# Kernel tuning notes

Measured on AMD Instinct MI355X. Metric: run time of the kernel, lower is better.

Reference implementation:

```python
import jax, jax.numpy as jnp
import numpy as np

NL, D, H, DH, DFF, DIN, MAXLEN = 3, 128, 4, 32, 512, 64, 4096
B, L = 2, 2048


def setup_inputs() -> dict:
    key = jax.random.key(0)
    ks = jax.random.split(key, 10)
    def n(k, shape, s=0.02):
        return jax.random.normal(k, shape, jnp.float32) * s
    return dict(
        x=jax.random.normal(ks[0], (B, L, DIN), jnp.float32),
        embed_w=n(ks[1], (D, DIN)), embed_b=jnp.zeros((D,), jnp.float32),
        pos_emb=n(ks[2], (MAXLEN + 1, D)),
        cls=n(ks[3], (1, 1, D)),
        in_proj_w=n(ks[4], (NL, 3 * D, D)), in_proj_b=jnp.zeros((NL, 3 * D), jnp.float32),
        out_w=n(ks[5], (NL, D, D)), out_b=jnp.zeros((NL, D), jnp.float32),
        ln1_s=jnp.ones((NL, D), jnp.float32), ln1_b=jnp.zeros((NL, D), jnp.float32),
        ln2_s=jnp.ones((NL, D), jnp.float32), ln2_b=jnp.zeros((NL, D), jnp.float32),
        ff1_w=n(ks[6], (NL, DFF, D)), ff1_b=jnp.zeros((NL, DFF), jnp.float32),
        ff2_w=n(ks[7], (NL, D, DFF)), ff2_b=jnp.zeros((NL, D), jnp.float32),
        head_ln_s=jnp.ones((D,), jnp.float32), head_ln_b=jnp.zeros((D,), jnp.float32),
        head_w=n(ks[8], (1, D)), head_b=jnp.zeros((1,), jnp.float32),
    )


def _ln(x, s, b, eps=1e-5):
    m = x.mean(-1, keepdims=True)
    v = ((x - m) ** 2).mean(-1, keepdims=True)
    return (x - m) * jax.lax.rsqrt(v + eps) * s + b


def reference(x, embed_w, embed_b, pos_emb, cls, in_proj_w, in_proj_b, out_w, out_b,
              ln1_s, ln1_b, ln2_s, ln2_b, ff1_w, ff1_b, ff2_w, ff2_b,
              head_ln_s, head_ln_b, head_w, head_b):
    b, l, _ = x.shape
    # token embedding + positional embeddings at indices 1..L (0 reserved for CLS)
    h = x @ embed_w.T + embed_b + pos_emb[1:l + 1]            # [B,L,D]
    cls_tok = jnp.broadcast_to(cls + pos_emb[0], (b, 1, D))   # CLS gets pos_emb[0]
    h = jnp.concatenate([cls_tok, h], axis=1)                 # [B,S,D], S=L+1
    s = l + 1
    scale = 1.0 / np.sqrt(DH).astype(np.float32)
    for i in range(NL):  # norm_first encoder layers, eager MHA (dropout=0 / eval)
        hn = _ln(h, ln1_s[i], ln1_b[i])
        qkv = hn @ in_proj_w[i].T + in_proj_b[i]
        q, k, v = jnp.split(qkv, 3, axis=-1)
        q = q.reshape(b, s, H, DH)
        k = k.reshape(b, s, H, DH)
        v = v.reshape(b, s, H, DH)
        attn = jax.nn.softmax(jnp.einsum('bqhd,bkhd->bhqk', q, k) * scale, axis=-1)
        o = jnp.einsum('bhqk,bkhd->bqhd', attn, v).reshape(b, s, D)
        h = h + o @ out_w[i].T + out_b[i]
        hn = _ln(h, ln2_s[i], ln2_b[i])
        h = h + jax.nn.relu(hn @ ff1_w[i].T + ff1_b[i]) @ ff2_w[i].T + ff2_b[i]
    pooled = _ln(h[:, 0], head_ln_s, head_ln_b)               # CLS pooling
    return (pooled @ head_w.T + head_b)[:, 0]                 # [B]
```

## Files before the change

### kernel.cpp

```cpp
#include <hip/hip_runtime.h>

typedef unsigned short u16;
typedef float f32x4 __attribute__((ext_vector_type(4)));
typedef short short8 __attribute__((ext_vector_type(8)));

#define S_LEN 2049
#define SPAD  2112
#define MP    4224
#define MT    264
#define MT32  132
#define KSPLIT 11

__device__ __forceinline__ float b2f(u16 u){
  unsigned int i = ((unsigned int)u) << 16; float f; __builtin_memcpy(&f, &i, 4); return f;
}
__device__ __forceinline__ u16 f2b(float f){
  unsigned int i; __builtin_memcpy(&i, &f, 4);
  unsigned int r = i + 0x7FFFu + ((i >> 16) & 1u);
  return (u16)(r >> 16);
}
__device__ __forceinline__ u16 f2b_fast(float f){
  unsigned int i; __builtin_memcpy(&i, &f, 4);
  return (u16)((i + 0x8000u) >> 16);
}
#if __has_builtin(__builtin_amdgcn_exp2f)
#define EXP2F(x) __builtin_amdgcn_exp2f(x)
#else
#define EXP2F(x) exp2f(x)
#endif

enum {
  OFF_X = 0,            OFF_EW = 262144,  OFF_EB = 270336,  OFF_POS = 270464,
  OFF_CLS = 794880,     OFF_IPW = 795008, OFF_IPB = 942464, OFF_OW = 943616,
  OFF_OB = 992768,      OFF_L1S = 993152, OFF_L1B = 993536, OFF_L2S = 993920,
  OFF_L2B = 994304,     OFF_F1W = 994688, OFF_F1B = 1191296, OFF_F2W = 1192832,
  OFF_F2B = 1389440,    OFF_HLS = 1389824, OFF_HLB = 1389952, OFF_HW = 1390080,
  OFF_HB = 1390208,     OFF_END = 1390209, CANON_PAD = 1390216
};

struct CArgs { const void* s[21]; };

__global__ __launch_bounds__(256) void init_kernel(
    CArgs a, u16* __restrict__ dst, float* __restrict__ h)
{
  const int offs[22] = {OFF_X,OFF_EW,OFF_EB,OFF_POS,OFF_CLS,OFF_IPW,OFF_IPB,OFF_OW,OFF_OB,
    OFF_L1S,OFF_L1B,OFF_L2S,OFF_L2B,OFF_F1W,OFF_F1B,OFF_F2W,OFF_F2B,OFF_HLS,OFF_HLB,
    OFF_HW,OFF_HB,OFF_END};
  int tid = blockIdx.x * 256 + threadIdx.x;
  if (tid < 256){
    int d = tid & 127, b = tid >> 7;
    h[(size_t)b * SPAD * 128 + d] =
        ((const float*)a.s[4])[d] + ((const float*)a.s[3])[d];
  }
  if (tid < 2 * 63 * 128){
    int b = tid / 8064, r = (tid % 8064) / 128, d = tid & 127;
    h[((size_t)b * SPAD + S_LEN + r) * 128 + d] = 0.f;
  }
  if (tid >= OFF_END) return;
  int lo = 0, hi = 21;
  while (hi - lo > 1){ int mid = (lo + hi) >> 1; if (tid >= offs[mid]) lo = mid; else hi = mid; }
  dst[tid] = f2b(((const float*)a.s[lo])[tid - offs[lo]]);
}

__global__ __launch_bounds__(256) void embed_kernel(const u16* __restrict__ cw, float* __restrict__ h)
{
  int lane = threadIdx.x & 63;
  int wave = blockIdx.x * 4 + (threadIdx.x >> 6);
  int mt = wave >> 3, nt = wave & 7;
  int mi = lane & 15, quad = lane >> 4;
  const u16* Ap = cw + OFF_X + (size_t)(mt * 16 + mi) * 64 + quad * 8;
  const u16* Wp = cw + OFF_EW + (size_t)(nt * 16 + mi) * 64 + quad * 8;
  f32x4 acc = {0.f, 0.f, 0.f, 0.f};
#pragma unroll
  for (int kc = 0; kc < 2; kc++){
    short8 av = *(const short8*)(Ap + kc * 32);
    short8 wv = *(const short8*)(Wp + kc * 32);
    acc = __builtin_amdgcn_mfma_f32_16x16x32_bf16(av, wv, acc, 0, 0, 0);
  }
  int n = nt * 16 + mi;
  float ebv = b2f(cw[OFF_EB + n]);
#pragma unroll
  for (int r = 0; r < 4; r++){
    int m = mt * 16 + quad * 4 + r;
    int b = m >> 11, s = (m & 2047) + 1;
    h[((size_t)b * SPAD + s) * 128 + n] =
        acc[r] + ebv + b2f(cw[OFF_POS + (size_t)s * 128 + n]);
  }
}

template<int N, int MODE>
__global__ __launch_bounds__(256) void lngemm_kernel(
    const float* __restrict__ h,
    const u16* __restrict__ g, const u16* __restrict__ be,
    const u16* __restrict__ W, const u16* __restrict__ bias, u16* __restrict__ out)
{
  constexpr int NT = N / 32;
  int lane = threadIdx.x & 63;
  int wave = blockIdx.x * 4 + (threadIdx.x >> 6);
  int mt = wave / NT, nt = wave - mt * NT;
  int mi = lane & 15, quad = lane >> 4;
  short8 af[2][4];
#pragma unroll
  for (int gi = 0; gi < 2; gi++){
    const float* hrow = h + (size_t)(mt * 32 + gi * 16 + mi) * 128 + quad * 8;
    float v[32];
    float sm = 0.f;
#pragma unroll
    for (int kc = 0; kc < 4; kc++){
      f32x4 x0 = *(const f32x4*)(hrow + kc * 32);
      f32x4 x1 = *(const f32x4*)(hrow + kc * 32 + 4);
#pragma unroll
      for (int j = 0; j < 4; j++){ v[kc*8+j] = x0[j]; v[kc*8+4+j] = x1[j]; }
      sm += x0[0]+x0[1]+x0[2]+x0[3]+x1[0]+x1[1]+x1[2]+x1[3];
    }
    sm += __shfl_xor(sm, 16, 64); sm += __shfl_xor(sm, 32, 64);
    float mean = sm * (1.f/128.f);
    float vv = 0.f;
#pragma unroll
    for (int j = 0; j < 32; j++){ float d = v[j] - mean; vv += d * d; }
    vv += __shfl_xor(vv, 16, 64); vv += __shfl_xor(vv, 32, 64);
    float rstd = rsqrtf(vv * (1.f/128.f) + 1e-5f);
#pragma unroll
    for (int kc = 0; kc < 4; kc++){
      short8 gs = *(const short8*)(g  + kc * 32 + quad * 8);
      short8 bs = *(const short8*)(be + kc * 32 + quad * 8);
#pragma unroll
      for (int j = 0; j < 8; j++)
        af[gi][kc][j] = (short)f2b((v[kc*8+j] - mean) * rstd * b2f((u16)gs[j]) + b2f((u16)bs[j]));
    }
  }
  const u16* W0 = W + (size_t)(nt * 32 + mi) * 128 + quad * 8;
  const u16* W1 = W0 + 16 * 128;
  f32x4 a00 = {0,0,0,0}, a01 = {0,0,0,0}, a10 = {0,0,0,0}, a11 = {0,0,0,0};
#pragma unroll
  for (int kc = 0; kc < 4; kc++){
    short8 w0 = *(const short8*)(W0 + kc * 32);
    short8 w1 = *(const short8*)(W1 + kc * 32);
    a00 = __builtin_amdgcn_mfma_f32_16x16x32_bf16(af[0][kc], w0, a00, 0, 0, 0);
    a01 = __builtin_amdgcn_mfma_f32_16x16x32_bf16(af[0][kc], w1, a01, 0, 0, 0);
    a10 = __builtin_amdgcn_mfma_f32_16x16x32_bf16(af[1][kc], w0, a10, 0, 0, 0);
    a11 = __builtin_amdgcn_mfma_f32_16x16x32_bf16(af[1][kc], w1, a11, 0, 0, 0);
  }
#pragma unroll
  for (int gi = 0; gi < 2; gi++){
#pragma unroll
    for (int wsel = 0; wsel < 2; wsel++){
      f32x4 acc = gi ? (wsel ? a11 : a10) : (wsel ? a01 : a00);
      int n = nt * 32 + wsel * 16 + mi;
      float bv = b2f(bias[n]);
#pragma unroll
      for (int r = 0; r < 4; r++){
        int m = mt * 32 + gi * 16 + quad * 4 + r;
        float val = acc[r] + bv;
        if (MODE == 0){
          int which = n >> 7, d = n & 127, hd = d >> 5, dh = d & 31;
          int b_ = (m >= SPAD) ? 1 : 0;
          int s  = m - b_ * SPAD;
          out[(size_t)(((which * 2 + b_) * 4 + hd) * SPAD + s) * 32 + dh] = f2b(val);
        } else {
          out[(size_t)m * N + n] = f2b(val > 0.f ? val : 0.f);
        }
      }
    }
  }
}

__global__ __launch_bounds__(256) void gemm_res_kernel(
    const u16* __restrict__ A, const u16* __restrict__ W, const u16* __restrict__ bias,
    float* __restrict__ hres)
{
  int lane = threadIdx.x & 63;
  int wave = blockIdx.x * 4 + (threadIdx.x >> 6);
  int mt = wave >> 2, nt = wave & 3;
  int mi = lane & 15, quad = lane >> 4;
  const u16* A0 = A + (size_t)(mt * 32 + mi) * 512 + quad * 8;
  const u16* A1 = A0 + 16 * 512;
  const u16* W0 = W + (size_t)(nt * 32 + mi) * 512 + quad * 8;
  const u16* W1 = W0 + 16 * 512;
  f32x4 a00 = {0,0,0,0}, a01 = {0,0,0,0}, a10 = {0,0,0,0}, a11 = {0,0,0,0};
#pragma unroll
  for (int kc = 0; kc < 16; kc++){
    short8 x0 = *(const short8*)(A0 + kc * 32);
    short8 x1 = *(const short8*)(A1 + kc * 32);
    short8 w0 = *(const short8*)(W0 + kc * 32);
    short8 w1 = *(const short8*)(W1 + kc * 32);
    a00 = __builtin_amdgcn_mfma_f32_16x16x32_bf16(x0, w0, a00, 0, 0, 0);
    a01 = __builtin_amdgcn_mfma_f32_16x16x32_bf16(x0, w1, a01, 0, 0, 0);
    a10 = __builtin_amdgcn_mfma_f32_16x16x32_bf16(x1, w0, a10, 0, 0, 0);
    a11 = __builtin_amdgcn_mfma_f32_16x16x32_bf16(x1, w1, a11, 0, 0, 0);
  }
#pragma unroll
  for (int gi = 0; gi < 2; gi++){
#pragma unroll
    for (int wsel = 0; wsel < 2; wsel++){
      f32x4 acc = gi ? (wsel ? a11 : a10) : (wsel ? a01 : a00);
      int n = nt * 32 + wsel * 16 + mi;
      float bv = b2f(bias[n]);
#pragma unroll
      for (int r = 0; r < 4; r++){
        int m = mt * 32 + gi * 16 + quad * 4 + r;
        hres[(size_t)m * 128 + n] += acc[r] + bv;
      }
    }
  }
}

__global__ __launch_bounds__(256, 4) void attn_kernel(
    const u16* __restrict__ qkv, float* __restrict__ Opart, float* __restrict__ Lpart)
{
  __shared__ u16 Kl[64 * 40];
  __shared__ u16 Vt[32 * 72];
  __shared__ u16 Pl[4][16 * 72];
  int tid = threadIdx.x;
  int lane = tid & 63, w = tid >> 6;
  int qt = blockIdx.x, bh = blockIdx.y, split = blockIdx.z;
  const u16* Qb = qkv + (size_t)bh * SPAD * 32;
  const u16* Kb = qkv + (size_t)(8 + bh) * SPAD * 32;
  const u16* Vb = qkv + (size_t)(16 + bh) * SPAD * 32;
  int mi = lane & 15, quad = lane >> 4;
  int q0 = qt * 64 + w * 16;
  short8 qf = *(const short8*)(Qb + (size_t)(q0 + mi) * 32 + quad * 8);
  f32x4 o0 = {0,0,0,0}, o1 = {0,0,0,0};
  float lp[4] = {0.f, 0.f, 0.f, 0.f};
  int c0 = split * 3, c1 = c0 + 3;
  int kkey = tid >> 2, kdh = (tid & 3) * 8;
  int vdh = tid & 31, vgrp = tid >> 5;
  u16* Pw = Pl[w];
  short8 kreg = *(const short8*)(Kb + (size_t)(c0 * 64 + kkey) * 32 + kdh);
  ushort4 va, vb;
  {
    const u16* vp = Vb + (size_t)(c0 * 64 + vgrp * 4) * 32 + vdh;
    va.x = vp[0];    va.y = vp[32];   va.z = vp[64];   va.w = vp[96];
    vb.x = vp[1024]; vb.y = vp[1056]; vb.z = vp[1088]; vb.w = vp[1120];
  }
  for (int c = c0; c < c1; c++){
    __syncthreads();
    *(short8*)&Kl[kkey * 40 + kdh] = kreg;
    *(ushort4*)&Vt[vdh * 72 + vgrp * 4] = va;
    *(ushort4*)&Vt[vdh * 72 + (vgrp + 8) * 4] = vb;
    {
      int cn = (c + 1 < c1) ? c + 1 : c;
      kreg = *(const short8*)(Kb + (size_t)(cn * 64 + kkey) * 32 + kdh);
      const u16* vp = Vb + (size_t)(cn * 64 + vgrp * 4) * 32 + vdh;
      va.x = vp[0];    va.y = vp[32];   va.z = vp[64];   va.w = vp[96];
      vb.x = vp[1024]; vb.y = vp[1056]; vb.z = vp[1088]; vb.w = vp[1120];
    }
    __syncthreads();
    int kb = c * 64;
#pragma unroll
    for (int kt = 0; kt < 4; kt++){
      short8 kf = *(const short8*)&Kl[(kt * 16 + mi) * 40 + quad * 8];
      f32x4 z = {0,0,0,0};
      f32x4 s = __builtin_amdgcn_mfma_f32_16x16x32_bf16(qf, kf, z, 0, 0, 0);
      bool val = (kb + kt * 16 + mi) < S_LEN;
#pragma unroll
      for (int r = 0; r < 4; r++){
        float p = val ? EXP2F(s[r] * 0.25503486f) : 0.f;
        lp[r] += p;
        Pw[(quad * 4 + r) * 72 + kt * 16 + mi] = f2b_fast(p);
      }
    }
    short8 pf0 = *(const short8*)&Pw[mi * 72 + quad * 8];
    short8 pf1 = *(const short8*)&Pw[mi * 72 + 32 + quad * 8];
    short8 wa0 = *(const short8*)&Vt[mi * 72 + quad * 8];
    short8 wa1 = *(const short8*)&Vt[mi * 72 + 32 + quad * 8];
    short8 wb0 = *(const short8*)&Vt[(16 + mi) * 72 + quad * 8];
    short8 wb1 = *(const short8*)&Vt[(16 + mi) * 72 + 32 + quad * 8];
    o0 = __builtin_amdgcn_mfma_f32_16x16x32_bf16(pf0, wa0, o0, 0, 0, 0);
    o0 = __builtin_amdgcn_mfma_f32_16x16x32_bf16(pf1, wa1, o0, 0, 0, 0);
    o1 = __builtin_amdgcn_mfma_f32_16x16x32_bf16(pf0, wb0, o1, 0, 0, 0);
    o1 = __builtin_amdgcn_mfma_f32_16x16x32_bf16(pf1, wb1, o1, 0, 0, 0);
  }
#pragma unroll
  for (int r = 0; r < 4; r++){
    lp[r] += __shfl_xor(lp[r], 1, 64); lp[r] += __shfl_xor(lp[r], 2, 64);
    lp[r] += __shfl_xor(lp[r], 4, 64); lp[r] += __shfl_xor(lp[r], 8, 64);
  }
  size_t pb = ((size_t)qt * 8 + bh) * KSPLIT + split;
  float* Ob = Opart + pb * 2048 + (size_t)w * 16 * 32;
#pragma unroll
  for (int r = 0; r < 4; r++){
    Ob[(quad * 4 + r) * 32 + mi]      = o0[r];
    Ob[(quad * 4 + r) * 32 + 16 + mi] = o1[r];
  }
  if (mi == 0){
#pragma unroll
    for (int r = 0; r < 4; r++)
      Lpart[pb * 64 + w * 16 + quad * 4 + r] = lp[r];
  }
}

__global__ __launch_bounds__(512, 2) void redout_kernel(
    const float* __restrict__ Opart, const float* __restrict__ Lpart,
    const u16* __restrict__ W, const u16* __restrict__ bias, float* __restrict__ hres)
{
  __shared__ u16 Al[16 * 136];
  int tid = threadIdx.x;
  int mt = blockIdx.x;
  int b = mt / 132, tle = mt % 132;
  int qt = tle >> 2, w = tle & 3;
  {
    int hd = tid >> 7;
    int e  = (tid * 4) & 511;
    int r  = e >> 5, dh0 = e & 31;
    size_t hb = ((size_t)qt * 8 + (b * 4 + hd)) * KSPLIT;
    size_t base = hb * 2048 + w * 512 + r * 32 + dh0;
    f32x4 acc = {0,0,0,0};
    float ls = 0.f;
#pragma unroll
    for (int sp = 0; sp < KSPLIT; sp++){
      acc += *(const f32x4*)(Opart + base + (size_t)sp * 2048);
      ls  += Lpart[(hb + sp) * 64 + w * 16 + r];
    }
    float inv = 1.f / fmaxf(ls, 1e-30f);
    ushort4 pk;
    pk.x = f2b(acc[0] * inv); pk.y = f2b(acc[1] * inv);
    pk.z = f2b(acc[2] * inv); pk.w = f2b(acc[3] * inv);
    *(ushort4*)&Al[r * 136 + hd * 32 + dh0] = pk;
  }
  __syncthreads();
  int lane = tid & 63, nt = tid >> 6;
  int mi = lane & 15, quad = lane >> 4;
  const u16* Wp = W + (size_t)(nt * 16 + mi) * 128 + quad * 8;
  f32x4 acc = {0.f, 0.f, 0.f, 0.f};
#pragma unroll
  for (int kc = 0; kc < 4; kc++){
    short8 af = *(const short8*)&Al[mi * 136 + kc * 32 + quad * 8];
    short8 wv = *(const short8*)(Wp + kc * 32);
    acc = __builtin_amdgcn_mfma_f32_16x16x32_bf16(af, wv, acc, 0, 0, 0);
  }
  int n = nt * 16 + mi;
  float bv = b2f(bias[n]);
#pragma unroll
  for (int r = 0; r < 4; r++){
    int m = mt * 16 + quad * 4 + r;
    hres[(size_t)m * 128 + n] += acc[r] + bv;
  }
}

__global__ __launch_bounds__(64) void head_kernel(
    const float* __restrict__ h, const u16* __restrict__ cw, float* __restrict__ out)
{
  int lane = threadIdx.x;
  for (int b = 0; b < 2; b++){
    float e0 = h[(size_t)b * SPAD * 128 + lane];
    float e1 = h[(size_t)b * SPAD * 128 + 64 + lane];
    float sm = e0 + e1;
    sm += __shfl_xor(sm,1,64); sm += __shfl_xor(sm,2,64); sm += __shfl_xor(sm,4,64);
    sm += __shfl_xor(sm,8,64); sm += __shfl_xor(sm,16,64); sm += __shfl_xor(sm,32,64);
    float mean = sm * (1.f/128.f);
    float d0 = e0 - mean, d1 = e1 - mean;
    float vv = d0*d0 + d1*d1;
    vv += __shfl_xor(vv,1,64); vv += __shfl_xor(vv,2,64); vv += __shfl_xor(vv,4,64);
    vv += __shfl_xor(vv,8,64); vv += __shfl_xor(vv,16,64); vv += __shfl_xor(vv,32,64);
    float rstd = rsqrtf(vv * (1.f/128.f) + 1e-5f);
    float v0 = d0 * rstd * b2f(cw[OFF_HLS + lane])      + b2f(cw[OFF_HLB + lane]);
    float v1 = d1 * rstd * b2f(cw[OFF_HLS + 64 + lane]) + b2f(cw[OFF_HLB + 64 + lane]);
    float dot = v0 * b2f(cw[OFF_HW + lane]) + v1 * b2f(cw[OFF_HW + 64 + lane]);
    dot += __shfl_xor(dot,1,64); dot += __shfl_xor(dot,2,64); dot += __shfl_xor(dot,4,64);
    dot += __shfl_xor(dot,8,64); dot += __shfl_xor(dot,16,64); dot += __shfl_xor(dot,32,64);
    if (lane == 0) out[b] = dot + b2f(cw[OFF_HB]);
  }
}

extern "C" void kernel_launch(void* const* d_in, const int* in_sizes, int n_in,
                              void* d_out, int out_size, void* d_ws, size_t ws_size,
                              hipStream_t stream)
{
  char* ws = (char*)d_ws;
  u16* cw     = (u16*)ws;    ws += (size_t)CANON_PAD * 2;
  float* h    = (float*)ws;  ws += (size_t)MP * 128 * 4;
  u16* qkv    = (u16*)ws;    ws += (size_t)24 * SPAD * 32 * 2;
  u16* f1     = (u16*)ws;    ws += (size_t)MP * 512 * 2;
  float* Opart= (float*)ws;  ws += (size_t)33 * 8 * KSPLIT * 2048 * 4;
  float* Lpart= (float*)ws;  ws += (size_t)33 * 8 * KSPLIT * 64 * 4;

  CArgs ca;
  for (int i = 0; i < 21; i++) ca.s[i] = d_in[i];

  init_kernel<<<dim3((OFF_END + 255) / 256), dim3(256), 0, stream>>>(ca, cw, h);
  embed_kernel<<<dim3(512), dim3(256), 0, stream>>>(cw, h);
  for (int l = 0; l < 3; l++){
    lngemm_kernel<384, 0><<<dim3(MT32 * 12 / 4), dim3(256), 0, stream>>>(
        h, cw + OFF_L1S + l * 128, cw + OFF_L1B + l * 128,
        cw + OFF_IPW + (size_t)l * 384 * 128, cw + OFF_IPB + l * 384, qkv);
    attn_kernel<<<dim3(33, 8, KSPLIT), dim3(256), 0, stream>>>(qkv, Opart, Lpart);
    redout_kernel<<<dim3(MT), dim3(512), 0, stream>>>(
        Opart, Lpart, cw + OFF_OW + (size_t)l * 128 * 128, cw + OFF_OB + l * 128, h);
    lngemm_kernel<512, 2><<<dim3(MT32 * 16 / 4), dim3(256), 0, stream>>>(
        h, cw + OFF_L2S + l * 128, cw + OFF_L2B + l * 128,
        cw + OFF_F1W + (size_t)l * 512 * 128, cw + OFF_F1B + l * 512, f1);
    gemm_res_kernel<<<dim3(MT32), dim3(256), 0, stream>>>(
        f1, cw + OFF_F2W + (size_t)l * 128 * 512, cw + OFF_F2B + l * 128, h);
  }
  head_kernel<<<dim3(1), dim3(64), 0, stream>>>(h, cw, (float*)d_out);
}
```

Measured before the change: 279.4 us.

## Fuse attention reduction, out-proj, LN2 and FF1; fuse FF2 with next-layer LN1+QKV

Replaces the separate redout, LN+FF1 GEMM, FF2 residual GEMM and LN+QKV GEMM kernels with two fused kernels per layer. Each one processes a 16-row tile: it updates the residual stream, keeps the tile in shared memory for the following LayerNorm, and runs the next projection. This cuts kernel launches and avoids re-reading h from global memory between stages. In exchange, row tiles shrink from 32 to 16, so more weight bytes are loaded per row, and each block's waves do their GEMM work serially behind barriers.

```diff
diff --git a/kernel.cpp b/kernel.cpp
--- a/kernel.cpp
+++ b/kernel.cpp
@@ -7,8 +7,7 @@
 #define S_LEN 2049
 #define SPAD  2112
 #define MP    4224
-#define MT    264
-#define MT32  132
+#define MT16  264
 #define KSPLIT 11
 
 __device__ __forceinline__ float b2f(u16 u){
@@ -88,118 +87,191 @@
   }
 }
 
-template<int N, int MODE>
-__global__ __launch_bounds__(256) void lngemm_kernel(
-    const float* __restrict__ h,
+__device__ __forceinline__ void ln_store(int tid, f32x4 x,
+    const u16* __restrict__ g, const u16* __restrict__ be, u16* __restrict__ Af)
+{
+  int row = tid >> 5, c = tid & 31;
+  float sm = x[0] + x[1] + x[2] + x[3];
+  sm += __shfl_xor(sm,1,64); sm += __shfl_xor(sm,2,64); sm += __shfl_xor(sm,4,64);
+  sm += __shfl_xor(sm,8,64); sm += __shfl_xor(sm,16,64);
+  float mean = sm * (1.f/128.f);
+  float d[4]; float vv = 0.f;
+#pragma unroll
+  for (int j = 0; j < 4; j++){ d[j] = x[j] - mean; vv += d[j]*d[j]; }
+  vv += __shfl_xor(vv,1,64); vv += __shfl_xor(vv,2,64); vv += __shfl_xor(vv,4,64);
+  vv += __shfl_xor(vv,8,64); vv += __shfl_xor(vv,16,64);
+  float rstd = rsqrtf(vv * (1.f/128.f) + 1e-5f);
+  ushort4 gv = *(const ushort4*)(g + c*4);
+  ushort4 bv = *(const ushort4*)(be + c*4);
+  ushort4 pk;
+  pk.x = f2b(d[0]*rstd*b2f(gv.x) + b2f(bv.x));
+  pk.y = f2b(d[1]*rstd*b2f(gv.y) + b2f(bv.y));
+  pk.z = f2b(d[2]*rstd*b2f(gv.z) + b2f(bv.z));
+  pk.w = f2b(d[3]*rstd*b2f(gv.w) + b2f(bv.w));
+  *(ushort4*)&Af[row*136 + c*4] = pk;
+}
+
+template<bool FF2, bool QKV>
+__global__ __launch_bounds__(512, 2) void fused_c_kernel(
+    float* __restrict__ h, const u16* __restrict__ f1,
+    const u16* __restrict__ f2w, const u16* __restrict__ f2bias,
     const u16* __restrict__ g, const u16* __restrict__ be,
-    const u16* __restrict__ W, const u16* __restrict__ bias, u16* __restrict__ out)
-{
-  constexpr int NT = N / 32;
-  int lane = threadIdx.x & 63;
-  int wave = blockIdx.x * 4 + (threadIdx.x >> 6);
-  int mt = wave / NT, nt = wave - mt * NT;
+    const u16* __restrict__ ipw, const u16* __restrict__ ipb,
+    u16* __restrict__ qkv)
+{
+  __shared__ float Ht[16 * 132];
+  __shared__ u16 Af[16 * 136];
+  int tid = threadIdx.x;
+  int lane = tid & 63, w = tid >> 6;
   int mi = lane & 15, quad = lane >> 4;
-  short8 af[2][4];
-#pragma unroll
-  for (int gi = 0; gi < 2; gi++){
-    const float* hrow = h + (size_t)(mt * 32 + gi * 16 + mi) * 128 + quad * 8;
-    float v[32];
-    float sm = 0.f;
+  int m0 = blockIdx.x * 16;
+  if (FF2){
+    int n0 = w * 16;
+    const u16* Ap = f1 + (size_t)(m0 + mi) * 512 + quad * 8;
+    const u16* Wp = f2w + (size_t)(n0 + mi) * 512 + quad * 8;
+    f32x4 acc = {0,0,0,0};
+#pragma unroll
+    for (int kc = 0; kc < 16; kc++){
+      short8 a = *(const short8*)(Ap + kc * 32);
+      short8 b = *(const short8*)(Wp + kc * 32);
+      acc = __builtin_amdgcn_mfma_f32_16x16x32_bf16(a, b, acc, 0, 0, 0);
+    }
+    int n = n0 + mi;
+    float bv = b2f(f2bias[n]);
+#pragma unroll
+    for (int r = 0; r < 4; r++){
+      int m = m0 + quad * 4 + r;
+      float val = h[(size_t)m * 128 + n] + acc[r] + bv;
+      h[(size_t)m * 128 + n] = val;
+      if (QKV) Ht[(quad * 4 + r) * 132 + n] = val;
+    }
+    if (QKV) __syncthreads();
+  }
+  if (QKV){
+    {
+      int row = tid >> 5, c = tid & 31;
+      f32x4 x;
+      if (FF2) x = *(const f32x4*)&Ht[row * 132 + c * 4];
+      else     x = *(const f32x4*)(h + (size_t)(m0 + row) * 128 + c * 4);
+      ln_store(tid, x, g, be, Af);
+    }
+    __syncthreads();
+    short8 af[4];
+#pragma unroll
+    for (int kc = 0; kc < 4; kc++)
+      af[kc] = *(const short8*)&Af[mi * 136 + kc * 32 + quad * 8];
+#pragma unroll
+    for (int t = 0; t < 3; t++){
+      int n0 = (w * 3 + t) * 16;
+      const u16* Wp = ipw + (size_t)(n0 + mi) * 128 + quad * 8;
+      f32x4 acc = {0,0,0,0};
+#pragma unroll
+      for (int kc = 0; kc < 4; kc++){
+        short8 wv = *(const short8*)(Wp + kc * 32);
+        acc = __builtin_amdgcn_mfma_f32_16x16x32_bf16(af[kc], wv, acc, 0, 0, 0);
+      }
+      int n = n0 + mi;
+      float bv = b2f(ipb[n]);
+      int which = n >> 7, d = n & 127, hd = d >> 5, dh = d & 31;
+#pragma unroll
+      for (int r = 0; r < 4; r++){
+        int m = m0 + quad * 4 + r;
+        int b_ = (m >= SPAD) ? 1 : 0;
+        int s  = m - b_ * SPAD;
+        qkv[(size_t)(((which * 2 + b_) * 4 + hd) * SPAD + s) * 32 + dh] = f2b(acc[r] + bv);
+      }
+    }
+  }
+}
+
+__global__ __launch_bounds__(512, 2) void fused_b_kernel(
+    const float* __restrict__ Opart, const float* __restrict__ Lpart,
+    const u16* __restrict__ ow, const u16* __restrict__ ob,
+    float* __restrict__ h,
+    const u16* __restrict__ g, const u16* __restrict__ be,
+    const u16* __restrict__ f1w, const u16* __restrict__ f1b,
+    u16* __restrict__ f1)
+{
+  __shared__ float Ht[16 * 132];
+  __shared__ u16 Af[16 * 136];
+  int tid = threadIdx.x;
+  int mt = blockIdx.x, m0 = mt * 16;
+  int b = mt / 132, tl = mt % 132;
+  int qt = tl >> 2, wq = tl & 3;
+  {
+    int r = tid >> 5, rem = tid & 31;
+    int hd = rem >> 3, dh0 = (rem & 7) * 4;
+    int q = wq * 16 + r;
+    size_t hb = ((size_t)qt * 8 + (b * 4 + hd)) * KSPLIT;
+    const float* Ob = Opart + hb * 2048 + q * 32 + dh0;
+    f32x4 acc = {0,0,0,0};
+    float ls = 0.f;
+#pragma unroll
+    for (int sp = 0; sp < KSPLIT; sp++){
+      acc += *(const f32x4*)(Ob + (size_t)sp * 2048);
+      ls  += Lpart[(hb + sp) * 64 + q];
+    }
+    float inv = 1.f / fmaxf(ls, 1e-30f);
+    ushort4 pk;
+    pk.x = f2b(acc[0]*inv); pk.y = f2b(acc[1]*inv);
+    pk.z = f2b(acc[2]*inv); pk.w = f2b(acc[3]*inv);
+    *(ushort4*)&Af[r * 136 + hd * 32 + dh0] = pk;
+  }
+  __syncthreads();
+  int lane = tid & 63, w = tid >> 6;
+  int mi = lane & 15, quad = lane >> 4;
+  {
+    short8 af[4];
+#pragma unroll
+    for (int kc = 0; kc < 4; kc++)
+      af[kc] = *(const short8*)&Af[mi * 136 + kc * 32 + quad * 8];
+    int n0 = w * 16;
+    const u16* Wp = ow + (size_t)(n0 + mi) * 128 + quad * 8;
+    f32x4 acc = {0,0,0,0};
 #pragma unroll
     for (int kc = 0; kc < 4; kc++){
-      f32x4 x0 = *(const f32x4*)(hrow + kc * 32);
-      f32x4 x1 = *(const f32x4*)(hrow + kc * 32 + 4);
-#pragma unroll
-      for (int j = 0; j < 4; j++){ v[kc*8+j] = x0[j]; v[kc*8+4+j] = x1[j]; }
-      sm += x0[0]+x0[1]+x0[2]+x0[3]+x1[0]+x1[1]+x1[2]+x1[3];
-    }
-    sm += __shfl_xor(sm, 16, 64); sm += __shfl_xor(sm, 32, 64);
-    float mean = sm * (1.f/128.f);
-    float vv = 0.f;
-#pragma unroll
-    for (int j = 0; j < 32; j++){ float d = v[j] - mean; vv += d * d; }
-    vv += __shfl_xor(vv, 16, 64); vv += __shfl_xor(vv, 32, 64);
-    float rstd = rsqrtf(vv * (1.f/128.f) + 1e-5f);
-#pragma unroll
-    for (int kc = 0; kc < 4; kc++){
-      short8 gs = *(const short8*)(g  + kc * 32 + quad * 8);
-      short8 bs = *(const short8*)(be + kc * 32 + quad * 8);
-#pragma unroll
-      for (int j = 0; j < 8; j++)
-        af[gi][kc][j] = (short)f2b((v[kc*8+j] - mean) * rstd * b2f((u16)gs[j]) + b2f((u16)bs[j]));
-    }
-  }
-  const u16* W0 = W + (size_t)(nt * 32 + mi) * 128 + quad * 8;
-  const u16* W1 = W0 + 16 * 128;
-  f32x4 a00 = {0,0,0,0}, a01 = {0,0,0,0}, a10 = {0,0,0,0}, a11 = {0,0,0,0};
-#pragma unroll
-  for (int kc = 0; kc < 4; kc++){
-    short8 w0 = *(const short8*)(W0 + kc * 32);
-    short8 w1 = *(const short8*)(W1 + kc * 32);
-    a00 = __builtin_amdgcn_mfma_f32_16x16x32_bf16(af[0][kc], w0, a00, 0, 0, 0);
-    a01 = __builtin_amdgcn_mfma_f32_16x16x32_bf16(af[0][kc], w1, a01, 0, 0, 0);
-    a10 = __builtin_amdgcn_mfma_f32_16x16x32_bf16(af[1][kc], w0, a10, 0, 0, 0);
-    a11 = __builtin_amdgcn_mfma_f32_16x16x32_bf16(af[1][kc], w1, a11, 0, 0, 0);
-  }
-#pragma unroll
-  for (int gi = 0; gi < 2; gi++){
-#pragma unroll
-    for (int wsel = 0; wsel < 2; wsel++){
-      f32x4 acc = gi ? (wsel ? a11 : a10) : (wsel ? a01 : a00);
-      int n = nt * 32 + wsel * 16 + mi;
-      float bv = b2f(bias[n]);
+      short8 wv = *(const short8*)(Wp + kc * 32);
+      acc = __builtin_amdgcn_mfma_f32_16x16x32_bf16(af[kc], wv, acc, 0, 0, 0);
+    }
+    int n = n0 + mi;
+    float bv = b2f(ob[n]);
+#pragma unroll
+    for (int r = 0; r < 4; r++){
+      int m = m0 + quad * 4 + r;
+      float val = h[(size_t)m * 128 + n] + acc[r] + bv;
+      h[(size_t)m * 128 + n] = val;
+      Ht[(quad * 4 + r) * 132 + n] = val;
+    }
+  }
+  __syncthreads();
+  {
+    int row = tid >> 5, c = tid & 31;
+    f32x4 x = *(const f32x4*)&Ht[row * 132 + c * 4];
+    ln_store(tid, x, g, be, Af);
+  }
+  __syncthreads();
+  {
+    short8 af[4];
+#pragma unroll
+    for (int kc = 0; kc < 4; kc++)
+      af[kc] = *(const short8*)&Af[mi * 136 + kc * 32 + quad * 8];
+#pragma unroll
+    for (int t = 0; t < 4; t++){
+      int n0 = (w * 4 + t) * 16;
+      const u16* Wp = f1w + (size_t)(n0 + mi) * 128 + quad * 8;
+      f32x4 acc = {0,0,0,0};
+#pragma unroll
+      for (int kc = 0; kc < 4; kc++){
+        short8 wv = *(const short8*)(Wp + kc * 32);
+        acc = __builtin_amdgcn_mfma_f32_16x16x32_bf16(af[kc], wv, acc, 0, 0, 0);
+      }
+      int n = n0 + mi;
+      float bv = b2f(f1b[n]);
 #pragma unroll
       for (int r = 0; r < 4; r++){
-        int m = mt * 32 + gi * 16 + quad * 4 + r;
+        int m = m0 + quad * 4 + r;
         float val = acc[r] + bv;
-        if (MODE == 0){
-          int which = n >> 7, d = n & 127, hd = d >> 5, dh = d & 31;
-          int b_ = (m >= SPAD) ? 1 : 0;
-          int s  = m - b_ * SPAD;
-          out[(size_t)(((which * 2 + b_) * 4 + hd) * SPAD + s) * 32 + dh] = f2b(val);
-        } else {
-          out[(size_t)m * N + n] = f2b(val > 0.f ? val : 0.f);
-        }
-      }
-    }
-  }
-}
-
-__global__ __launch_bounds__(256) void gemm_res_kernel(
-    const u16* __restrict__ A, const u16* __restrict__ W, const u16* __restrict__ bias,
-    float* __restrict__ hres)
-{
-  int lane = threadIdx.x & 63;
-  int wave = blockIdx.x * 4 + (threadIdx.x >> 6);
-  int mt = wave >> 2, nt = wave & 3;
-  int mi = lane & 15, quad = lane >> 4;
-  const u16* A0 = A + (size_t)(mt * 32 + mi) * 512 + quad * 8;
-  const u16* A1 = A0 + 16 * 512;
-  const u16* W0 = W + (size_t)(nt * 32 + mi) * 512 + quad * 8;
-  const u16* W1 = W0 + 16 * 512;
-  f32x4 a00 = {0,0,0,0}, a01 = {0,0,0,0}, a10 = {0,0,0,0}, a11 = {0,0,0,0};
-#pragma unroll
-  for (int kc = 0; kc < 16; kc++){
-    short8 x0 = *(const short8*)(A0 + kc * 32);
-    short8 x1 = *(const short8*)(A1 + kc * 32);
-    short8 w0 = *(const short8*)(W0 + kc * 32);
-    short8 w1 = *(const short8*)(W1 + kc * 32);
-    a00 = __builtin_amdgcn_mfma_f32_16x16x32_bf16(x0, w0, a00, 0, 0, 0);
-    a01 = __builtin_amdgcn_mfma_f32_16x16x32_bf16(x0, w1, a01, 0, 0, 0);
-    a10 = __builtin_amdgcn_mfma_f32_16x16x32_bf16(x1, w0, a10, 0, 0, 0);
-    a11 = __builtin_amdgcn_mfma_f32_16x16x32_bf16(x1, w1, a11, 0, 0, 0);
-  }
-#pragma unroll
-  for (int gi = 0; gi < 2; gi++){
-#pragma unroll
-    for (int wsel = 0; wsel < 2; wsel++){
-      f32x4 acc = gi ? (wsel ? a11 : a10) : (wsel ? a01 : a00);
-      int n = nt * 32 + wsel * 16 + mi;
-      float bv = b2f(bias[n]);
-#pragma unroll
-      for (int r = 0; r < 4; r++){
-        int m = mt * 32 + gi * 16 + quad * 4 + r;
-        hres[(size_t)m * 128 + n] += acc[r] + bv;
+        f1[(size_t)m * 512 + n] = f2b(val > 0.f ? val : 0.f);
       }
     }
   }
@@ -290,54 +362,6 @@
   }
 }
 
-__global__ __launch_bounds__(512, 2) void redout_kernel(
-    const float* __restrict__ Opart, const float* __restrict__ Lpart,
-    const u16* __restrict__ W, const u16* __restrict__ bias, float* __restrict__ hres)
-{
-  __shared__ u16 Al[16 * 136];
-  int tid = threadIdx.x;
-  int mt = blockIdx.x;
-  int b = mt / 132, tle = mt % 132;
-  int qt = tle >> 2, w = tle & 3;
-  {
-    int hd = tid >> 7;
-    int e  = (tid * 4) & 511;
-    int r  = e >> 5, dh0 = e & 31;
-    size_t hb = ((size_t)qt * 8 + (b * 4 + hd)) * KSPLIT;
-    size_t base = hb * 2048 + w * 512 + r * 32 + dh0;
-    f32x4 acc = {0,0,0,0};
-    float ls = 0.f;
-#pragma unroll
-    for (int sp = 0; sp < KSPLIT; sp++){
-      acc += *(const f32x4*)(Opart + base + (size_t)sp * 2048);
-      ls  += Lpart[(hb + sp) * 64 + w * 16 + r];
-    }
-    float inv = 1.f / fmaxf(ls, 1e-30f);
-    ushort4 pk;
-    pk.x = f2b(acc[0] * inv); pk.y = f2b(acc[1] * inv);
-    pk.z = f2b(acc[2] * inv); pk.w = f2b(acc[3] * inv);
-    *(ushort4*)&Al[r * 136 + hd * 32 + dh0] = pk;
-  }
-  __syncthreads();
-  int lane = tid & 63, nt = tid >> 6;
-  int mi = lane & 15, quad = lane >> 4;
-  const u16* Wp = W + (size_t)(nt * 16 + mi) * 128 + quad * 8;
-  f32x4 acc = {0.f, 0.f, 0.f, 0.f};
-#pragma unroll
-  for (int kc = 0; kc < 4; kc++){
-    short8 af = *(const short8*)&Al[mi * 136 + kc * 32 + quad * 8];
-    short8 wv = *(const short8*)(Wp + kc * 32);
-    acc = __builtin_amdgcn_mfma_f32_16x16x32_bf16(af, wv, acc, 0, 0, 0);
-  }
-  int n = nt * 16 + mi;
-  float bv = b2f(bias[n]);
-#pragma unroll
-  for (int r = 0; r < 4; r++){
-    int m = mt * 16 + quad * 4 + r;
-    hres[(size_t)m * 128 + n] += acc[r] + bv;
-  }
-}
-
 __global__ __launch_bounds__(64) void head_kernel(
     const float* __restrict__ h, const u16* __restrict__ cw, float* __restrict__ out)
 {
@@ -380,18 +404,25 @@
 
   init_kernel<<<dim3((OFF_END + 255) / 256), dim3(256), 0, stream>>>(ca, cw, h);
   embed_kernel<<<dim3(512), dim3(256), 0, stream>>>(cw, h);
+  fused_c_kernel<false, true><<<dim3(MT16), dim3(512), 0, stream>>>(
+      h, nullptr, nullptr, nullptr,
+      cw + OFF_L1S, cw + OFF_L1B, cw + OFF_IPW, cw + OFF_IPB, qkv);
   for (int l = 0; l < 3; l++){
-    lngemm_kernel<384, 0><<<dim3(MT32 * 12 / 4), dim3(256), 0, stream>>>(
-        h, cw + OFF_L1S + l * 128, cw + OFF_L1B + l * 128,
-        cw + OFF_IPW + (size_t)l * 384 * 128, cw + OFF_IPB + l * 384, qkv);
     attn_kernel<<<dim3(33, 8, KSPLIT), dim3(256), 0, stream>>>(qkv, Opart, Lpart);
-    redout_kernel<<<dim3(MT), dim3(512), 0, stream>>>(
-        Opart, Lpart, cw + OFF_OW + (size_t)l * 128 * 128, cw + OFF_OB + l * 128, h);
-    lngemm_kernel<512, 2><<<dim3(MT32 * 16 / 4), dim3(256), 0, stream>>>(
-        h, cw + OFF_L2S + l * 128, cw + OFF_L2B + l * 128,
+    fused_b_kernel<<<dim3(MT16), dim3(512), 0, stream>>>(
+        Opart, Lpart, cw + OFF_OW + (size_t)l * 128 * 128, cw + OFF_OB + l * 128, h,
+        cw + OFF_L2S + l * 128, cw + OFF_L2B + l * 128,
         cw + OFF_F1W + (size_t)l * 512 * 128, cw + OFF_F1B + l * 512, f1);
-    gemm_res_kernel<<<dim3(MT32), dim3(256), 0, stream>>>(
-        f1, cw + OFF_F2W + (size_t)l * 128 * 512, cw + OFF_F2B + l * 128, h);
+    if (l < 2){
+      fused_c_kernel<true, true><<<dim3(MT16), dim3(512), 0, stream>>>(
+          h, f1, cw + OFF_F2W + (size_t)l * 128 * 512, cw + OFF_F2B + l * 128,
+          cw + OFF_L1S + (l+1) * 128, cw + OFF_L1B + (l+1) * 128,
+          cw + OFF_IPW + (size_t)(l+1) * 384 * 128, cw + OFF_IPB + (l+1) * 384, qkv);
+    } else {
+      fused_c_kernel<true, false><<<dim3(MT16), dim3(512), 0, stream>>>(
+          h, f1, cw + OFF_F2W + (size_t)l * 128 * 512, cw + OFF_F2B + l * 128,
+          nullptr, nullptr, nullptr, nullptr, nullptr);
+    }
   }
   head_kernel<<<dim3(1), dim3(64), 0, stream>>>(h, cw, (float*)d_out);
 }
```

Result: slower. 287.2 us (+2.8%).
